# Kernel tuning notes

Hardware: AMD Instinct MI355X
Metric: run time of the kernel (lower is better)

Reference implementation:

```python
import jax, jax.numpy as jnp
import numpy as np

EPS = 1e-12


def _pchip_slopes(y, x):
    """PCHIP (Fritsch-Carlson) slopes. y: (S, K), x: (K) -> (S, K)."""
    K = y.shape[-1]
    if K < 2:
        return jnp.zeros_like(y)
    h = x[1:] - x[:-1]                              # (K-1,)
    delta = (y[..., 1:] - y[..., :-1]) / (h + EPS)  # (S, K-1)
    if K == 2:
        return jnp.broadcast_to(delta[..., :1], y.shape).astype(y.dtype)
    # interior slopes: weighted harmonic mean where secants agree in sign
    delta_prev = delta[..., :-1]
    delta_next = delta[..., 1:]
    same_sign = delta_prev * delta_next > 0
    h_prev = h[:-1]
    h_next = h[1:]
    w1 = 2.0 * h_next + h_prev
    w2 = h_next + 2.0 * h_prev
    denom = w1 / (delta_prev + EPS) + w2 / (delta_next + EPS)
    d_int = (w1 + w2) / (denom + EPS)
    d_mid = jnp.where(same_sign, d_int, jnp.zeros_like(d_int))  # (S, K-2)
    # left endpoint (one-sided, shape-limited)
    h0, h1 = h[0], h[1]
    delta0 = delta[..., 0]
    delta1 = delta[..., 1]
    d0 = ((2.0 * h0 + h1) * delta0 - h0 * delta1) / (h0 + h1 + EPS)
    d0 = jnp.where(jnp.sign(d0) != jnp.sign(delta0), jnp.zeros_like(d0), d0)
    d0 = jnp.where((jnp.sign(delta0) != jnp.sign(delta1)) & (jnp.abs(d0) > 3.0 * jnp.abs(delta0)), 3.0 * delta0, d0)
    # right endpoint
    hn1, hn2 = h[-1], h[-2]
    deltan1 = delta[..., -1]
    deltan2 = delta[..., -2]
    dn = ((2.0 * hn1 + hn2) * deltan1 - hn1 * deltan2) / (hn1 + hn2 + EPS)
    dn = jnp.where(jnp.sign(dn) != jnp.sign(deltan1), jnp.zeros_like(dn), dn)
    dn = jnp.where((jnp.sign(deltan1) != jnp.sign(deltan2)) & (jnp.abs(dn) > 3.0 * jnp.abs(deltan1)), 3.0 * deltan1, dn)
    return jnp.concatenate([d0[..., None], d_mid, dn[..., None]], axis=-1)


def setup_inputs() -> dict:
    key = jax.random.key(0)
    k1, k2 = jax.random.split(key)
    B, S, K = 4096, 4096, 64
    x_min, x_max = -3.0, 3.0
    xq = jax.random.normal(k1, (B, S), dtype=jnp.float32) * 2.0  # some queries outside domain
    coeffs = jax.random.normal(k2, (S, K), dtype=jnp.float32)
    knots = jnp.linspace(x_min, x_max, K, dtype=jnp.float32)
    return {"xq": xq, "coeffs": coeffs, "knots": knots}


def reference(xq, coeffs, knots):
    y = coeffs                                   # (S, K)
    d = _pchip_slopes(y, knots)                  # (S, K)
    K = knots.shape[0]
    x0_dom = knots[0]
    x1_dom = knots[-1]
    below = xq < x0_dom
    above = xq > x1_dom
    xq_c = jnp.clip(xq, x0_dom, x1_dom)
    idx = jnp.searchsorted(knots, xq_c) - 1      # (B, S) interval index
    idx = jnp.clip(idx, 0, K - 2)
    x0 = knots[idx]
    x1 = knots[idx + 1]
    h = x1 - x0 + EPS
    t = (xq_c - x0) / h
    t2 = t * t
    t3 = t2 * t
    h00 = 2.0 * t3 - 3.0 * t2 + 1.0
    h10 = t3 - 2.0 * t2 + t
    h01 = -2.0 * t3 + 3.0 * t2
    h11 = t3 - t2
    s_idx = jnp.arange(y.shape[0])[None, :]      # (1, S) spline index
    y0 = y[s_idx, idx]
    y1 = y[s_idx, idx + 1]
    d0 = d[s_idx, idx]
    d1 = d[s_idx, idx + 1]
    interp = h00 * y0 + h10 * h * d0 + h01 * y1 + h11 * h * d1
    out = jnp.where(below, y[None, :, 0] + d[None, :, 0] * (xq - x0_dom), interp)
    out = jnp.where(above, y[None, :, -1] + d[None, :, -1] * (xq - x1_dom), out)
    return out
```

## Files before the change

### kernel.cpp

```cpp
#include <hip/hip_runtime.h>

#define EPSF 1e-12f
#define STILE 64
#define KK 64
#define LSTR 65
#define PLANE (STILE * LSTR)
#define BLK 512
#define UNROLL 8

__device__ __forceinline__ float sgnf(float x) {
    return (x > 0.f) ? 1.f : ((x < 0.f) ? -1.f : 0.f);
}

__global__ __launch_bounds__(BLK, 4) void pchip_fused2(
    const float* __restrict__ xq,
    const float* __restrict__ coeffs,
    const float* __restrict__ knots,
    float* __restrict__ out,
    int S, int b_chunk)
{
    __shared__ float pl[4 * PLANE];
    __shared__ float skn[KK];

    int tid = threadIdx.x;
    int s0 = blockIdx.x * STILE;
    int b0 = blockIdx.y * b_chunk;

    float* p0 = pl;
    float* p1 = pl + PLANE;
    float* p2 = pl + 2 * PLANE;
    float* p3 = pl + 3 * PLANE;

    if (tid < KK) skn[tid] = knots[tid];
#pragma unroll
    for (int i = 0; i < (STILE * KK) / BLK; i++) {
        int p = tid + i * BLK;
        int sl = p >> 6, k = p & 63;
        p0[sl * LSTR + k] = coeffs[(size_t)(s0 + sl) * KK + k];
    }
    __syncthreads();
#pragma unroll
    for (int i = 0; i < (STILE * KK) / BLK; i++) {
        int p = tid + i * BLK;
        int sl = p >> 6, k = p & 63;
        if (k < KK - 1) {
            float h = skn[k + 1] - skn[k];
            p3[sl * LSTR + k] = (p0[sl * LSTR + k + 1] - p0[sl * LSTR + k]) / (h + EPSF);
        }
    }
    __syncthreads();
    float dreg[(STILE * KK) / BLK];
#pragma unroll
    for (int i = 0; i < (STILE * KK) / BLK; i++) {
        int p = tid + i * BLK;
        int sl = p >> 6, k = p & 63;
        const float* del = p3 + sl * LSTR;
        float d;
        if (k == 0) {
            float h0 = skn[1] - skn[0], h1 = skn[2] - skn[1];
            float de0 = del[0], de1 = del[1];
            d = ((2.f * h0 + h1) * de0 - h0 * de1) / (h0 + h1 + EPSF);
            if (sgnf(d) != sgnf(de0)) d = 0.f;
            if ((sgnf(de0) != sgnf(de1)) && (fabsf(d) > 3.f * fabsf(de0))) d = 3.f * de0;
        } else if (k == KK - 1) {
            float hn1 = skn[KK - 1] - skn[KK - 2], hn2 = skn[KK - 2] - skn[KK - 3];
            float dn1 = del[KK - 2], dn2 = del[KK - 3];
            d = ((2.f * hn1 + hn2) * dn1 - hn1 * dn2) / (hn1 + hn2 + EPSF);
            if (sgnf(d) != sgnf(dn1)) d = 0.f;
            if ((sgnf(dn1) != sgnf(dn2)) && (fabsf(d) > 3.f * fabsf(dn1))) d = 3.f * dn1;
        } else {
            float dprev = del[k - 1], dnext = del[k];
            float hp = skn[k] - skn[k - 1], hn = skn[k + 1] - skn[k];
            bool same = dprev * dnext > 0.f;
            float w1 = 2.f * hn + hp;
            float w2 = hn + 2.f * hp;
            float denom = w1 / (dprev + EPSF) + w2 / (dnext + EPSF);
            float dint = (w1 + w2) / (denom + EPSF);
            d = same ? dint : 0.f;
        }
        dreg[i] = d;
    }
    __syncthreads();
#pragma unroll
    for (int i = 0; i < (STILE * KK) / BLK; i++) {
        int p = tid + i * BLK;
        int sl = p >> 6, k = p & 63;
        p2[sl * LSTR + k] = dreg[i];
    }
    __syncthreads();
    float c1r[(STILE * KK) / BLK], c2r[(STILE * KK) / BLK], c3r[(STILE * KK) / BLK];
#pragma unroll
    for (int i = 0; i < (STILE * KK) / BLK; i++) {
        int p = tid + i * BLK;
        int sl = p >> 6, k = p & 63;
        int kc = min(k, KK - 2);
        int ib = sl * LSTR + kc;
        float y0 = p0[ib], y1 = p0[ib + 1];
        float d0 = p2[ib], d1 = p2[ib + 1];
        float h = skn[kc + 1] - skn[kc] + EPSF;
        c1r[i] = h * d0;
        c2r[i] = 3.f * (y1 - y0) - h * (2.f * d0 + d1);
        c3r[i] = 2.f * (y0 - y1) + h * (d0 + d1);
    }
    __syncthreads();
#pragma unroll
    for (int i = 0; i < (STILE * KK) / BLK; i++) {
        int p = tid + i * BLK;
        int sl = p >> 6, k = p & 63;
        if (k < KK - 1) {
            int ib = sl * LSTR + k;
            p1[ib] = c1r[i];
            p2[ib] = c2r[i];
            p3[ib] = c3r[i];
        }
    }
    __syncthreads();

    float x0d = skn[0], x1d = skn[KK - 1];
    float invh = (float)(KK - 1) / (x1d - x0d);
    float af = invh, bf = -x0d * invh;
    int wave = tid >> 6, lane = tid & 63;
    const float* q0 = p0 + lane * LSTR;
    const float* q1 = p1 + lane * LSTR;
    const float* q2 = p2 + lane * LSTR;
    const float* q3 = p3 + lane * LSTR;

    int rows_per_wave = b_chunk >> 3;
    size_t off0 = (size_t)(b0 + wave * rows_per_wave) * S + s0 + lane;
    for (int ii = 0; ii < rows_per_wave; ii += UNROLL) {
        float xv[UNROLL];
#pragma unroll
        for (int j = 0; j < UNROLL; j++) xv[j] = xq[off0 + (size_t)j * S];
        float rv[UNROLL];
#pragma unroll
        for (int j = 0; j < UNROLL; j++) {
            float x = xv[j];
            float tf = fmaf(x, af, bf);
            float tcf = fminf(fmaxf(tf, 0.f), (float)(KK - 1));
            int idx = min((int)tcf, KK - 2);
            float t = tcf - (float)idx;
            float c0 = q0[idx], c1 = q1[idx], c2 = q2[idx], c3 = q3[idx];
            float P = fmaf(fmaf(fmaf(c3, t, c2), t, c1), t, c0);
            float w = fmaf(fmaf(t, 2.f, t), c3, c2 + c2);
            float Pp = fmaf(t, w, c1);
            float ext = tf - tcf;
            rv[j] = fmaf(Pp, ext, P);
        }
#pragma unroll
        for (int j = 0; j < UNROLL; j++) out[off0 + (size_t)j * S] = rv[j];
        off0 += (size_t)UNROLL * S;
    }
}

extern "C" void kernel_launch(void* const* d_in, const int* in_sizes, int n_in,
                              void* d_out, int out_size, void* d_ws, size_t ws_size,
                              hipStream_t stream) {
    const float* xq     = (const float*)d_in[0];
    const float* coeffs = (const float*)d_in[1];
    const float* knots  = (const float*)d_in[2];
    float* out = (float*)d_out;

    int K = in_sizes[2];
    int S = in_sizes[1] / K;
    int N = in_sizes[0];
    int B = N / S;

    int n_btiles = 8;
    int b_chunk = B / n_btiles;
    dim3 grid(S / STILE, n_btiles);
    pchip_fused2<<<grid, BLK, 0, stream>>>(xq, coeffs, knots, out, S, b_chunk);
}
```

Baseline: 125.5 us.

## Interleave spline coefficients as float4 in LDS and vectorize query loads

Stores the four cubic coefficients per interval interleaved as one float4 in shared memory, so each query does a single 128-bit LDS read instead of four scalar reads. Doubles the block to 1024 threads, has each lane handle two adjacent splines using float2 global loads and stores, and drops one setup sync by writing slopes straight into shared memory. LDS footprint is about the same, but the float4 gather across lanes spaced two rows apart may cause bank conflicts, and launch bounds of 1024x8 may limit registers.

```diff
diff --git a/kernel.cpp b/kernel.cpp
--- a/kernel.cpp
+++ b/kernel.cpp
@@ -3,73 +3,84 @@
 #define EPSF 1e-12f
 #define STILE 64
 #define KK 64
-#define LSTR 65
-#define PLANE (STILE * LSTR)
-#define BLK 512
-#define UNROLL 8
+#define RSTR 65
+#define FSTR (4 * RSTR)
+#define BLK 1024
+#define NWAVE (BLK / 64)
+#define PRELOOP ((STILE * KK) / BLK)
+#define UNROLL 4
 
 __device__ __forceinline__ float sgnf(float x) {
     return (x > 0.f) ? 1.f : ((x < 0.f) ? -1.f : 0.f);
 }
 
-__global__ __launch_bounds__(BLK, 4) void pchip_fused2(
+__device__ __forceinline__ float eval1(float x, const float4* __restrict__ q,
+                                       float af, float bf) {
+    float tf = fmaf(x, af, bf);
+    float tcf = fminf(fmaxf(tf, 0.f), (float)(KK - 1));
+    int idx = min((int)tcf, KK - 2);
+    float t = tcf - (float)idx;
+    float4 c = q[idx];
+    float P = fmaf(fmaf(fmaf(c.w, t, c.z), t, c.y), t, c.x);
+    float w = fmaf(fmaf(t, 2.f, t), c.w, c.z + c.z);
+    float Pp = fmaf(t, w, c.y);
+    return fmaf(Pp, tf - tcf, P);
+}
+
+__global__ __launch_bounds__(BLK, 8) void pchip_fused3(
     const float* __restrict__ xq,
     const float* __restrict__ coeffs,
     const float* __restrict__ knots,
     float* __restrict__ out,
     int S, int b_chunk)
 {
-    __shared__ float pl[4 * PLANE];
+    __shared__ float4 cf4[STILE * RSTR];
     __shared__ float skn[KK];
+    float* cf = (float*)cf4;
 
     int tid = threadIdx.x;
     int s0 = blockIdx.x * STILE;
     int b0 = blockIdx.y * b_chunk;
 
-    float* p0 = pl;
-    float* p1 = pl + PLANE;
-    float* p2 = pl + 2 * PLANE;
-    float* p3 = pl + 3 * PLANE;
-
     if (tid < KK) skn[tid] = knots[tid];
 #pragma unroll
-    for (int i = 0; i < (STILE * KK) / BLK; i++) {
+    for (int i = 0; i < PRELOOP; i++) {
         int p = tid + i * BLK;
         int sl = p >> 6, k = p & 63;
-        p0[sl * LSTR + k] = coeffs[(size_t)(s0 + sl) * KK + k];
+        cf[sl * FSTR + 4 * k] = coeffs[(size_t)(s0 + sl) * KK + k];
     }
     __syncthreads();
 #pragma unroll
-    for (int i = 0; i < (STILE * KK) / BLK; i++) {
+    for (int i = 0; i < PRELOOP; i++) {
         int p = tid + i * BLK;
         int sl = p >> 6, k = p & 63;
         if (k < KK - 1) {
-            float h = skn[k + 1] - skn[k];
-            p3[sl * LSTR + k] = (p0[sl * LSTR + k + 1] - p0[sl * LSTR + k]) / (h + EPSF);
+            int ib = sl * FSTR + 4 * k;
+            float hh = skn[k + 1] - skn[k];
+            cf[ib + 3] = (cf[ib + 4] - cf[ib]) / (hh + EPSF);
         }
     }
     __syncthreads();
-    float dreg[(STILE * KK) / BLK];
 #pragma unroll
-    for (int i = 0; i < (STILE * KK) / BLK; i++) {
+    for (int i = 0; i < PRELOOP; i++) {
         int p = tid + i * BLK;
         int sl = p >> 6, k = p & 63;
-        const float* del = p3 + sl * LSTR;
+        int rb = sl * FSTR;
         float d;
         if (k == 0) {
             float h0 = skn[1] - skn[0], h1 = skn[2] - skn[1];
-            float de0 = del[0], de1 = del[1];
+            float de0 = cf[rb + 3], de1 = cf[rb + 7];
             d = ((2.f * h0 + h1) * de0 - h0 * de1) / (h0 + h1 + EPSF);
             if (sgnf(d) != sgnf(de0)) d = 0.f;
             if ((sgnf(de0) != sgnf(de1)) && (fabsf(d) > 3.f * fabsf(de0))) d = 3.f * de0;
         } else if (k == KK - 1) {
             float hn1 = skn[KK - 1] - skn[KK - 2], hn2 = skn[KK - 2] - skn[KK - 3];
-            float dn1 = del[KK - 2], dn2 = del[KK - 3];
+            float dn1 = cf[rb + 4 * (KK - 2) + 3], dn2 = cf[rb + 4 * (KK - 3) + 3];
             d = ((2.f * hn1 + hn2) * dn1 - hn1 * dn2) / (hn1 + hn2 + EPSF);
             if (sgnf(d) != sgnf(dn1)) d = 0.f;
             if ((sgnf(dn1) != sgnf(dn2)) && (fabsf(d) > 3.f * fabsf(dn1))) d = 3.f * dn1;
         } else {
-            float dprev = del[k - 1], dnext = del[k];
+            float dprev = cf[rb + 4 * (k - 1) + 3], dnext = cf[rb + 4 * k + 3];
             float hp = skn[k] - skn[k - 1], hn = skn[k + 1] - skn[k];
             bool same = dprev * dnext > 0.f;
             float w1 = 2.f * hn + hp;
@@ -78,25 +89,18 @@
             float dint = (w1 + w2) / (denom + EPSF);
             d = same ? dint : 0.f;
         }
-        dreg[i] = d;
+        cf[rb + 4 * k + 2] = d;
     }
     __syncthreads();
+    float c1r[PRELOOP], c2r[PRELOOP], c3r[PRELOOP];
 #pragma unroll
-    for (int i = 0; i < (STILE * KK) / BLK; i++) {
-        int p = tid + i * BLK;
-        int sl = p >> 6, k = p & 63;
-        p2[sl * LSTR + k] = dreg[i];
-    }
-    __syncthreads();
-    float c1r[(STILE * KK) / BLK], c2r[(STILE * KK) / BLK], c3r[(STILE * KK) / BLK];
-#pragma unroll
-    for (int i = 0; i < (STILE * KK) / BLK; i++) {
+    for (int i = 0; i < PRELOOP; i++) {
         int p = tid + i * BLK;
         int sl = p >> 6, k = p & 63;
         int kc = min(k, KK - 2);
-        int ib = sl * LSTR + kc;
-        float y0 = p0[ib], y1 = p0[ib + 1];
-        float d0 = p2[ib], d1 = p2[ib + 1];
+        int ib = sl * FSTR + 4 * kc;
+        float y0 = cf[ib], y1 = cf[ib + 4];
+        float d0 = cf[ib + 2], d1 = cf[ib + 6];
         float h = skn[kc + 1] - skn[kc] + EPSF;
         c1r[i] = h * d0;
         c2r[i] = 3.f * (y1 - y0) - h * (2.f * d0 + d1);
@@ -104,14 +108,14 @@
     }
     __syncthreads();
 #pragma unroll
-    for (int i = 0; i < (STILE * KK) / BLK; i++) {
+    for (int i = 0; i < PRELOOP; i++) {
         int p = tid + i * BLK;
         int sl = p >> 6, k = p & 63;
         if (k < KK - 1) {
-            int ib = sl * LSTR + k;
-            p1[ib] = c1r[i];
-            p2[ib] = c2r[i];
-            p3[ib] = c3r[i];
+            int ib = sl * FSTR + 4 * k;
+            cf[ib + 1] = c1r[i];
+            cf[ib + 2] = c2r[i];
+            cf[ib + 3] = c3r[i];
         }
     }
     __syncthreads();
@@ -120,35 +124,27 @@
     float invh = (float)(KK - 1) / (x1d - x0d);
     float af = invh, bf = -x0d * invh;
     int wave = tid >> 6, lane = tid & 63;
-    const float* q0 = p0 + lane * LSTR;
-    const float* q1 = p1 + lane * LSTR;
-    const float* q2 = p2 + lane * LSTR;
-    const float* q3 = p3 + lane * LSTR;
+    int brow = lane >> 5;
+    int scol = (lane & 31) << 1;
+    const float4* q0 = cf4 + scol * RSTR;
+    const float4* q1 = q0 + RSTR;
 
-    int rows_per_wave = b_chunk >> 3;
-    size_t off0 = (size_t)(b0 + wave * rows_per_wave) * S + s0 + lane;
-    for (int ii = 0; ii < rows_per_wave; ii += UNROLL) {
-        float xv[UNROLL];
+    int rows_per_wave = b_chunk / NWAVE;
+    size_t off0 = (size_t)(b0 + wave * rows_per_wave + brow) * S + s0 + scol;
+    int nb = rows_per_wave >> 1;
+    for (int ii = 0; ii < nb; ii += UNROLL) {
+        float2 xv[UNROLL];
 #pragma unroll
-        for (int j = 0; j < UNROLL; j++) xv[j] = xq[off0 + (size_t)j * S];
-        float rv[UNROLL];
+        for (int j = 0; j < UNROLL; j++)
+            xv[j] = *(const float2*)(xq + off0 + (size_t)(2 * j) * S);
 #pragma unroll
         for (int j = 0; j < UNROLL; j++) {
-            float x = xv[j];
-            float tf = fmaf(x, af, bf);
-            float tcf = fminf(fmaxf(tf, 0.f), (float)(KK - 1));
-            int idx = min((int)tcf, KK - 2);
-            float t = tcf - (float)idx;
-            float c0 = q0[idx], c1 = q1[idx], c2 = q2[idx], c3 = q3[idx];
-            float P = fmaf(fmaf(fmaf(c3, t, c2), t, c1), t, c0);
-            float w = fmaf(fmaf(t, 2.f, t), c3, c2 + c2);
-            float Pp = fmaf(t, w, c1);
-            float ext = tf - tcf;
-            rv[j] = fmaf(Pp, ext, P);
+            float2 r;
+            r.x = eval1(xv[j].x, q0, af, bf);
+            r.y = eval1(xv[j].y, q1, af, bf);
+            *(float2*)(out + off0 + (size_t)(2 * j) * S) = r;
         }
-#pragma unroll
-        for (int j = 0; j < UNROLL; j++) out[off0 + (size_t)j * S] = rv[j];
-        off0 += (size_t)UNROLL * S;
+        off0 += (size_t)(2 * UNROLL) * S;
     }
 }
 
@@ -168,5 +164,5 @@
     int n_btiles = 8;
     int b_chunk = B / n_btiles;
     dim3 grid(S / STILE, n_btiles);
-    pchip_fused2<<<grid, BLK, 0, stream>>>(xq, coeffs, knots, out, S, b_chunk);
+    pchip_fused3<<<grid, BLK, 0, stream>>>(xq, coeffs, knots, out, S, b_chunk);
 }
```

Measured after the change: 125.8 us. About the same (+0.2%).
